# Kernel tuning notes

Measured on AMD Instinct MI355X. Metric: run time of the kernel, lower is better.

## Reference

```python
import jax, jax.numpy as jnp
import numpy as np

B, T = 64, 128
IN, H, L, OUT = 512, 1024, 2, 1


def _gru_scan(seq, Wi, Wh, bi, bh):
    # seq: (S, in_dim); PyTorch GRU cell, gate order r, z, n.
    h0 = jnp.zeros((H,), dtype=seq.dtype)
    def step(h, x):
        gi = x @ Wi.T + bi          # (3H,)
        gh = h @ Wh.T + bh          # (3H,)
        r = jax.nn.sigmoid(gi[:H] + gh[:H])
        z = jax.nn.sigmoid(gi[H:2 * H] + gh[H:2 * H])
        n = jnp.tanh(gi[2 * H:] + r * gh[2 * H:])
        h_new = (1.0 - z) * n + z * h
        return h_new, h_new
    _, hs = jax.lax.scan(step, h0, seq)
    return hs                        # (S, H)


def setup_inputs() -> dict:
    key = jax.random.key(0)
    ks = jax.random.split(key, 24)
    mk = lambda k, shape: jax.random.normal(k, shape, dtype=jnp.float32) * 0.05
    d = {}
    d['x'] = jax.random.normal(ks[0], (B, T, IN), dtype=jnp.float32)
    # gru1: layer0 input=IN, layer1 input=H
    d['g1_Wi0'] = mk(ks[1], (3 * H, IN)); d['g1_Wh0'] = mk(ks[2], (3 * H, H))
    d['g1_bi0'] = mk(ks[3], (3 * H,));    d['g1_bh0'] = mk(ks[4], (3 * H,))
    d['g1_Wi1'] = mk(ks[5], (3 * H, H));  d['g1_Wh1'] = mk(ks[6], (3 * H, H))
    d['g1_bi1'] = mk(ks[7], (3 * H,));    d['g1_bh1'] = mk(ks[8], (3 * H,))
    # gru2: both layers input=H
    d['g2_Wi0'] = mk(ks[9], (3 * H, H));  d['g2_Wh0'] = mk(ks[10], (3 * H, H))
    d['g2_bi0'] = mk(ks[11], (3 * H,));   d['g2_bh0'] = mk(ks[12], (3 * H,))
    d['g2_Wi1'] = mk(ks[13], (3 * H, H)); d['g2_Wh1'] = mk(ks[14], (3 * H, H))
    d['g2_bi1'] = mk(ks[15], (3 * H,));   d['g2_bh1'] = mk(ks[16], (3 * H,))
    d['fc1_W'] = mk(ks[17], (64, H));     d['fc1_b'] = mk(ks[18], (64,))
    d['fc2_W'] = mk(ks[19], (OUT, 64));   d['fc2_b'] = mk(ks[20], (OUT,))
    return d


def reference(x, g1_Wi0, g1_Wh0, g1_bi0, g1_bh0, g1_Wi1, g1_Wh1, g1_bi1, g1_bh1,
              g2_Wi0, g2_Wh0, g2_bi0, g2_bh0, g2_Wi1, g2_Wh1, g2_bi1, g2_bh1,
              fc1_W, fc1_b, fc2_W, fc2_b):
    # PyTorch feeds x[:, t, :] (2-D) to a batch_first GRU -> treated as an
    # UNBATCHED sequence of length B; hidden is carried across t. That equals
    # one GRU scan over the flattened (T*B)-step sequence, t-major / b-minor.
    seq = jnp.swapaxes(x, 0, 1).reshape(T * B, IN)
    hs0 = _gru_scan(seq, g1_Wi0, g1_Wh0, g1_bi0, g1_bh0)    # (T*B, H) layer 0
    hs1 = _gru_scan(hs0, g1_Wi1, g1_Wh1, g1_bi1, g1_bh1)    # (T*B, H) layer 1
    # h returned after timestep t is the hidden at flat step t*B + (B-1)
    s = jnp.stack([hs0, hs1], axis=1)[B - 1::B]             # (T, L, H)
    seq2 = s.reshape(T * L, H)                              # torch.cat(s)
    # gru2 over the [1, T*L, H] sequence (batch=1)
    hs2_0 = _gru_scan(seq2, g2_Wi0, g2_Wh0, g2_bi0, g2_bh0)
    hs2_1 = _gru_scan(hs2_0, g2_Wi1, g2_Wh1, g2_bi1, g2_bh1)
    h2 = jnp.stack([hs2_0[-1], hs2_1[-1]], axis=0)[:, None, :]  # (L, 1, H)
    y = jax.nn.sigmoid(h2 @ fc1_W.T + fc1_b)                # (L, 1, 64)
    out = jax.nn.sigmoid(y @ fc2_W.T + fc2_b)               # (L, 1, OUT)
    return out
```

## Files before the change

kernel.cpp:

```cpp
#include <hip/hip_runtime.h>


typedef unsigned u32x4 __attribute__((ext_vector_type(4)));
typedef unsigned u32x2 __attribute__((ext_vector_type(2)));
typedef _Float16 h2_t  __attribute__((ext_vector_type(2)));

#define NWG 256

__device__ u32x4    g_recL0[2][NWG];
__device__ u32x4    g_recL1[2][NWG];
__device__ unsigned g_seq2[256][512];

__device__ __forceinline__ unsigned pk(float a, float b) {
  unsigned short ua = __builtin_bit_cast(unsigned short, (_Float16)a);
  unsigned short ub = __builtin_bit_cast(unsigned short, (_Float16)b);
  return (unsigned)ua | ((unsigned)ub << 16);
}
__device__ __forceinline__ float unpk(unsigned u, int hi) {
  unsigned short us = (unsigned short)(hi ? (u >> 16) : (u & 0xffffu));
  return (float)__builtin_bit_cast(_Float16, us);
}

#if __has_builtin(__builtin_amdgcn_fdot2)
__device__ __forceinline__ float fdot2(unsigned a, unsigned b, float c) {
  return __builtin_amdgcn_fdot2(__builtin_bit_cast(h2_t, a),
                                __builtin_bit_cast(h2_t, b), c, false);
}
#else
__device__ __forceinline__ float fdot2(unsigned a, unsigned b, float c) {
  h2_t ha = __builtin_bit_cast(h2_t, a), hb = __builtin_bit_cast(h2_t, b);
  return c + (float)ha[0] * (float)hb[0] + (float)ha[1] * (float)hb[1];
}
#endif

__device__ __forceinline__ u32x4 ld_sc_v4(const u32x4* p) {
  u32x4 v;
  asm volatile("global_load_dwordx4 %0, %1, off sc1\n\t"
               "s_waitcnt vmcnt(0)"
               : "=&v"(v) : "v"(p) : "memory");
  return v;
}
__device__ __forceinline__ void st_sc_v4(u32x4* p, u32x4 v) {
  asm volatile("global_store_dwordx4 %0, %1, off sc1"
               :: "v"(p), "v"(v) : "memory");
}
__device__ __forceinline__ void st_sc_v2(void* p, u32x2 v) {
  asm volatile("global_store_dwordx2 %0, %1, off sc1"
               :: "v"(p), "v"(v) : "memory");
}

__device__ __forceinline__ float rcpf(float x) {
#if __has_builtin(__builtin_amdgcn_rcpf)
  return __builtin_amdgcn_rcpf(x);
#else
  return 1.f / x;
#endif
}
__device__ __forceinline__ float sigf(float x) {
  return rcpf(1.f + __expf(-x));
}
__device__ __forceinline__ float tanh_f(float x) {
  x = fminf(fmaxf(x, -15.f), 15.f);
  const float e = __expf(2.f * x);
  return (e - 1.f) * rcpf(e + 1.f);
}

__device__ __forceinline__ int swzHc(int ch) { return ch ^ ((ch >> 3) & 7); }
__device__ __forceinline__ int swzXc(int ch) { return ch ^ ((ch >> 2) & 7); }
__device__ __forceinline__ int swzH_pos(int idx) { return (swzHc(idx >> 2) << 2) | (idx & 3); }
__device__ __forceinline__ int swzX_pos(int idx) { return (swzXc(idx >> 2) << 2) | (idx & 3); }

__global__ void init_recs() {
  int t = blockIdx.x * blockDim.x + threadIdx.x;
  u32x4 ff = {0u, 0u, 0xFFFFFFFFu, 0u};
  if (t < 512)       g_recL0[t >> 8][t & 255] = ff;
  else               g_recL1[(t - 512) >> 8][t & 255] = ff;
}

#define LDROW16(T, A, B, C, D)                                                 \
  {                                                                            \
    const int rr = g4 * 3 + (T);                                               \
    const float4* r4 = (const float4*)(Wm + (size_t)((rr >> 2) * 1024 + j0 +   \
                       (rr & 3)) * cols + kh * (cols >> 1) + q * (cols >> 5)); \
    float4 v;                                                                  \
    v = r4[0]; A[0] = pk(v.x, v.y); A[1] = pk(v.z, v.w);                       \
    v = r4[1]; A[2] = pk(v.x, v.y); A[3] = pk(v.z, v.w);                       \
    v = r4[2]; B[0] = pk(v.x, v.y); B[1] = pk(v.z, v.w);                       \
    v = r4[3]; B[2] = pk(v.x, v.y); B[3] = pk(v.z, v.w);                       \
    v = r4[4]; C[0] = pk(v.x, v.y); C[1] = pk(v.z, v.w);                       \
    v = r4[5]; C[2] = pk(v.x, v.y); C[3] = pk(v.z, v.w);                       \
    v = r4[6]; D[0] = pk(v.x, v.y); D[1] = pk(v.z, v.w);                       \
    v = r4[7]; D[2] = pk(v.x, v.y); D[3] = pk(v.z, v.w);                       \
  }

#define LDROW8(T, A, B)                                                        \
  {                                                                            \
    const int rr = g4 * 3 + (T);                                               \
    const float4* r4 = (const float4*)(Wm + (size_t)((rr >> 2) * 1024 + j0 +   \
                       (rr & 3)) * cols + kh * (cols >> 1) + q * (cols >> 5)); \
    float4 v;                                                                  \
    v = r4[0]; A[0] = pk(v.x, v.y); A[1] = pk(v.z, v.w);                       \
    v = r4[1]; A[2] = pk(v.x, v.y); A[3] = pk(v.z, v.w);                       \
    v = r4[2]; B[0] = pk(v.x, v.y); B[1] = pk(v.z, v.w);                       \
    v = r4[3]; B[2] = pk(v.x, v.y); B[3] = pk(v.z, v.w);                       \
  }

#define DOTK(HSRC, IDX, A, B, C)                                               \
  {                                                                            \
    u32x4 h4 = HSRC[(IDX)];                                                    \
    acc0 = fdot2(A[0], h4[0], acc0); acc0 = fdot2(A[1], h4[1], acc0);          \
    acc0 = fdot2(A[2], h4[2], acc0); acc0 = fdot2(A[3], h4[3], acc0);          \
    acc1 = fdot2(B[0], h4[0], acc1); acc1 = fdot2(B[1], h4[1], acc1);          \
    acc1 = fdot2(B[2], h4[2], acc1); acc1 = fdot2(B[3], h4[3], acc1);          \
    acc2 = fdot2(C[0], h4[0], acc2); acc2 = fdot2(C[1], h4[1], acc2);          \
    acc2 = fdot2(C[2], h4[2], acc2); acc2 = fdot2(C[3], h4[3], acc2);          \
  }

template <int PHASE>
__global__ __launch_bounds__(512, 2) void gru_phase(
    const float* __restrict__ Wm0, const float* __restrict__ Wm1,
    const float* __restrict__ Wm2, const float* __restrict__ Wm3,
    const float* __restrict__ bh0, const float* __restrict__ bi1,
    const float* __restrict__ bh1, const float* __restrict__ bi0,
    const float* __restrict__ x,
    const float* __restrict__ fc1W, const float* __restrict__ fc1b,
    const float* __restrict__ fc2W, const float* __restrict__ fc2b,
    float* __restrict__ out)
{
  constexpr int N0 = (PHASE == 1) ? 8192 : 256;
  constexpr int XC = (PHASE == 1) ? 512 : 1024;

  const int wg   = blockIdx.x;
  const int tid  = threadIdx.x;
  const int wv   = tid >> 6;
  const int lane = tid & 63;
  const int m    = wv >> 1;
  const int kh   = wv & 1;
  const int g4   = lane >> 4;
  const int q    = lane & 15;
  const int j0   = wg * 4;
  const bool m3s = (PHASE == 1) && (m == 3);

  __shared__ __attribute__((aligned(16))) unsigned sH0[2][512];
  __shared__ __attribute__((aligned(16))) unsigned sH1[2][512];
  __shared__ __attribute__((aligned(16))) unsigned sX [2][512];
  __shared__ float sD[2][96];
  __shared__ float sY[128];

  u32x4 W0{}, W1{}, W2{}, W3{}, W4{}, W5{}, W6{}, W7{}, W8{}, W9{}, W10{}, W11{};
  {
    const float* Wm = (m == 0) ? Wm0 : (m == 1) ? Wm1 : (m == 2) ? Wm2 : Wm3;
    const int cols = (m == 3) ? XC : 1024;
    if (m3s) {
      LDROW8(0, W0, W1);
      LDROW8(1, W2, W3);
      LDROW8(2, W4, W5);
    } else {
      LDROW16(0, W0, W4, W8,  W2);
      LDROW16(0, W0, W1, W2,  W3);
      LDROW16(1, W4, W5, W6,  W7);
      LDROW16(2, W8, W9, W10, W11);
    }
  }

  float bI0, bI1, bI2, bH0v, bH1v, bH2v;
  {
    const int i = lane & 3, layer = (lane >> 2) & 1;
    const float* pbi = layer ? bi1 : bi0;
    const float* pbh = layer ? bh1 : bh0;
    bI0 = pbi[0 * 1024 + j0 + i]; bI1 = pbi[1 * 1024 + j0 + i]; bI2 = pbi[2 * 1024 + j0 + i];
    bH0v = pbh[0 * 1024 + j0 + i]; bH1v = pbh[1 * 1024 + j0 + i]; bH2v = pbh[2 * 1024 + j0 + i];
  }

  for (int s = 0; s <= N0; ++s) {
    const int par = s & 1;

    float2 xv = {0.f, 0.f};
    unsigned xs = 0;
    if (PHASE == 1) {
      if (s < N0 && tid < 256) {
        const int b = s & 63, tt = s >> 6;
        xv = ((const float2*)(x + (size_t)(b * 128 + tt) * 512))[tid];
      }
    } else {
      if (s < N0) xs = g_seq2[s][tid];
    }

    const int t2 = tid & 255;
    {
      unsigned d0 = 0, d1 = 0;
      if (s > 0) {
        const unsigned want = (unsigned)(s - 1);
        const u32x4* a = (tid < 256) ? &g_recL0[(s - 1) & 1][t2]
                                     : &g_recL1[(s - 1) & 1][t2];
        u32x4 r = ld_sc_v4(a);
        while (r[2] != want) r = ld_sc_v4(a);
        d0 = r[0]; d1 = r[1];
      }
      unsigned* dst = (tid < 256) ? sH0[par] : sH1[par];
      dst[swzH_pos(2 * t2)]     = d0;
      dst[swzH_pos(2 * t2 + 1)] = d1;
    }
    if (PHASE == 1) {
      if (s < N0 && tid < 256) sX[par][swzX_pos(tid)] = pk(xv.x, xv.y);
    } else {
      if (s < N0) sX[par][swzH_pos(tid)] = xs;
    }
    __syncthreads();

    float acc0 = 0.f, acc1 = 0.f, acc2 = 0.f;
    if (m3s) {
      const u32x4* Xv = (const u32x4*)sX[par];
      const int base = kh * 32 + 2 * q;
      DOTK(Xv, swzXc(base + 0), W0, W2, W4);
      DOTK(Xv, swzXc(base + 1), W1, W3, W5);
    } else {
      const unsigned* hb = (m == 2) ? sH1[par] : (m == 3) ? sX[par] : sH0[par];
      const u32x4* Hv = (const u32x4*)hb;
      const int base = kh * 64 + 4 * q;
      DOTK(Hv, swzHc(base + 0), W0, W4, W8);
      DOTK(Hv, swzHc(base + 1), W1, W5, W9);
      DOTK(Hv, swzHc(base + 2), W2, W6, W10);
      DOTK(Hv, swzHc(base + 3), W3, W7, W11);
    }
    acc0 += __shfl_xor(acc0, 8, 16); acc0 += __shfl_xor(acc0, 4, 16);
    acc0 += __shfl_xor(acc0, 2, 16); acc0 += __shfl_xor(acc0, 1, 16);
    acc1 += __shfl_xor(acc1, 8, 16); acc1 += __shfl_xor(acc1, 4, 16);
    acc1 += __shfl_xor(acc1, 2, 16); acc1 += __shfl_xor(acc1, 1, 16);
    acc2 += __shfl_xor(acc2, 8, 16); acc2 += __shfl_xor(acc2, 4, 16);
    acc2 += __shfl_xor(acc2, 2, 16); acc2 += __shfl_xor(acc2, 1, 16);
    if (q < 3) {
      const float dv = (q == 0) ? acc0 : (q == 1) ? acc1 : acc2;
      sD[par][m * 24 + kh * 12 + g4 * 3 + q] = dv;
    }
    __syncthreads();

    if (wv == 0) {
      const int i = lane & 3;
      const int layer = (lane >> 2) & 1;
      const float* Sd = sD[par];
      const int mI = layer ? 1 : 3;
      const int mH = layer ? 2 : 0;
      const float dIr = Sd[mI * 24 + 0 + i] + Sd[mI * 24 + 12 + 0 + i];
      const float dIz = Sd[mI * 24 + 4 + i] + Sd[mI * 24 + 12 + 4 + i];
      const float dIn = Sd[mI * 24 + 8 + i] + Sd[mI * 24 + 12 + 8 + i];
      const float dHr = Sd[mH * 24 + 0 + i] + Sd[mH * 24 + 12 + 0 + i];
      const float dHz = Sd[mH * 24 + 4 + i] + Sd[mH * 24 + 12 + 4 + i];
      const float dHn = Sd[mH * 24 + 8 + i] + Sd[mH * 24 + 12 + 8 + i];
      const float rg = sigf(dIr + bI0 + dHr + bH0v);
      const float zg = sigf(dIz + bI1 + dHz + bH1v);
      const float ng = tanh_f(dIn + bI2 + rg * (dHn + bH2v));
      const int   jj = 2 * wg + (i >> 1);
      const unsigned hu = (layer ? sH1 : sH0)[par][swzH_pos(jj)];
      const float hp = unpk(hu, i & 1);
      float hn = (1.f - zg) * ng + zg * hp;
      const bool valid = layer ? (s >= 1) : (s < N0);
      hn = valid ? hn : 0.f;
      const float v0 = __shfl(hn, 0), v1 = __shfl(hn, 1);
      const float v2 = __shfl(hn, 2), v3 = __shfl(hn, 3);
      const float w0 = __shfl(hn, 4), w1 = __shfl(hn, 5);
      const float w2 = __shfl(hn, 6), w3 = __shfl(hn, 7);
      if (lane == 0) {
        u32x4 rec0 = {pk(v0, v1), pk(v2, v3), (unsigned)s, 0u};
        u32x4 rec1 = {pk(w0, w1), pk(w2, w3), (unsigned)s, 0u};
        st_sc_v4(&g_recL0[par][wg], rec0);
        st_sc_v4(&g_recL1[par][wg], rec1);
        if (PHASE == 1) {
          if ((s & 63) == 63) {
            u32x2 t2v = {rec0[0], rec0[1]};
            st_sc_v2(&g_seq2[2 * (s >> 6)][2 * wg], t2v);
          }
          if (s >= 1 && ((s - 1) & 63) == 63) {
            u32x2 t2v = {rec1[0], rec1[1]};
            st_sc_v2(&g_seq2[2 * ((s - 1) >> 6) + 1][2 * wg], t2v);
          }
        }
      }
    }
  }

  if (PHASE == 2 && wg == 0) {
    if (tid < 256) {
      const u32x4* a1 = &g_recL1[0][tid];
      u32x4 r1 = ld_sc_v4(a1);
      while (r1[2] != 256u) r1 = ld_sc_v4(a1);
      sH1[0][swzH_pos(2 * tid)]     = r1[0];
      sH1[0][swzH_pos(2 * tid + 1)] = r1[1];
    }
    __syncthreads();
    if (tid < 128) {
      const int lsel = tid >> 6;
      const int k = tid & 63;
      const unsigned* Hs = lsel ? sH1[0] : sH0[0];
      const float* wrow = fc1W + (size_t)k * 1024;
      float a = fc1b[k];
      for (int j2 = 0; j2 < 512; ++j2) {
        const unsigned hu = Hs[swzH_pos(j2)];
        a += unpk(hu, 0) * wrow[2 * j2] + unpk(hu, 1) * wrow[2 * j2 + 1];
      }
      sY[tid] = sigf(a);
    }
    __syncthreads();
    if (tid < 2) {
      const float* yv = sY + tid * 64;
      float a = fc2b[0];
      for (int k2 = 0; k2 < 64; ++k2) a += fc2W[k2] * yv[k2];
      out[tid] = sigf(a);
    }
  }
}

extern "C" void kernel_launch(void* const* d_in, const int* in_sizes, int n_in,
                              void* d_out, int out_size, void* d_ws, size_t ws_size,
                              hipStream_t stream) {
  (void)in_sizes; (void)n_in; (void)out_size; (void)d_ws; (void)ws_size;
  const float* x      = (const float*)d_in[0];
  const float* g1_Wi0 = (const float*)d_in[1];
  const float* g1_Wh0 = (const float*)d_in[2];
  const float* g1_bi0 = (const float*)d_in[3];
  const float* g1_bh0 = (const float*)d_in[4];
  const float* g1_Wi1 = (const float*)d_in[5];
  const float* g1_Wh1 = (const float*)d_in[6];
  const float* g1_bi1 = (const float*)d_in[7];
  const float* g1_bh1 = (const float*)d_in[8];
  const float* g2_Wi0 = (const float*)d_in[9];
  const float* g2_Wh0 = (const float*)d_in[10];
  const float* g2_bi0 = (const float*)d_in[11];
  const float* g2_bh0 = (const float*)d_in[12];
  const float* g2_Wi1 = (const float*)d_in[13];
  const float* g2_Wh1 = (const float*)d_in[14];
  const float* g2_bi1 = (const float*)d_in[15];
  const float* g2_bh1 = (const float*)d_in[16];
  const float* fc1W   = (const float*)d_in[17];
  const float* fc1b   = (const float*)d_in[18];
  const float* fc2W   = (const float*)d_in[19];
  const float* fc2b   = (const float*)d_in[20];
  float* out = (float*)d_out;

  init_recs<<<dim3(4), dim3(256), 0, stream>>>();
  gru_phase<1><<<dim3(NWG), dim3(512), 0, stream>>>(
      g1_Wh0, g1_Wi1, g1_Wh1, g1_Wi0, g1_bh0, g1_bi1, g1_bh1, g1_bi0,
      x, fc1W, fc1b, fc2W, fc2b, out);
  gru_phase<2><<<dim3(NWG), dim3(512), 0, stream>>>(
      g2_Wh0, g2_Wi1, g2_Wh1, g2_Wi0, g2_bh0, g2_bi1, g2_bh1, g2_bi0,
      x, fc1W, fc1b, fc2W, fc2b, out);
}
```

Measured before the change: 26.75 ms.

## Relay cross-step hidden state through one elected block per XCD

Elects one workgroup per XCC with an atomic CAS to act as a relay. The relay polls the system-coherent recurrence buffers and copies the records into a per-XCC mirror held at L2 scope. Other workgroups spin on that L2-local mirror instead, with an occasional fallback poll of the global buffer. The aim is to cut cross-die coherent polling traffic and latency in the per-step barrier, at the cost of an extra hop through the relay and more init work. It also removes a redundant duplicate weight-load macro.

```diff
diff --git a/kernel.cpp b/kernel.cpp
--- a/kernel.cpp
+++ b/kernel.cpp
@@ -9,6 +9,8 @@
 
 __device__ u32x4    g_recL0[2][NWG];
 __device__ u32x4    g_recL1[2][NWG];
+__device__ u32x4    g_mirror[8][2][512];
+__device__ int      g_relay[8];
 __device__ unsigned g_seq2[256][512];
 
 __device__ __forceinline__ unsigned pk(float a, float b) {
@@ -40,8 +42,19 @@
                : "=&v"(v) : "v"(p) : "memory");
   return v;
 }
+__device__ __forceinline__ u32x4 ld_l2_v4(const u32x4* p) {
+  u32x4 v;
+  asm volatile("global_load_dwordx4 %0, %1, off sc0\n\t"
+               "s_waitcnt vmcnt(0)"
+               : "=&v"(v) : "v"(p) : "memory");
+  return v;
+}
 __device__ __forceinline__ void st_sc_v4(u32x4* p, u32x4 v) {
   asm volatile("global_store_dwordx4 %0, %1, off sc1"
+               :: "v"(p), "v"(v) : "memory");
+}
+__device__ __forceinline__ void st_l2_v4(u32x4* p, u32x4 v) {
+  asm volatile("global_store_dwordx4 %0, %1, off sc0"
                :: "v"(p), "v"(v) : "memory");
 }
 __device__ __forceinline__ void st_sc_v2(void* p, u32x2 v) {
@@ -73,8 +86,10 @@
 __global__ void init_recs() {
   int t = blockIdx.x * blockDim.x + threadIdx.x;
   u32x4 ff = {0u, 0u, 0xFFFFFFFFu, 0u};
-  if (t < 512)       g_recL0[t >> 8][t & 255] = ff;
-  else               g_recL1[(t - 512) >> 8][t & 255] = ff;
+  if (t < 512)              g_recL0[t >> 8][t & 255] = ff;
+  else if (t < 1024)        g_recL1[(t - 512) >> 8][t & 255] = ff;
+  else if (t < 1024 + 8192) ((u32x4*)g_mirror)[t - 1024] = ff;
+  if (t < 8) g_relay[t] = -1;
 }
 
 #define LDROW16(T, A, B, C, D)                                                 \
@@ -146,6 +161,15 @@
   __shared__ __attribute__((aligned(16))) unsigned sX [2][512];
   __shared__ float sD[2][96];
   __shared__ float sY[128];
+  __shared__ int   sRole;
+
+  unsigned xcc;
+  asm volatile("s_getreg_b32 %0, hwreg(HW_REG_XCC_ID)" : "=s"(xcc));
+  xcc &= 7u;
+  if (tid == 0) {
+    int old = atomicCAS(&g_relay[xcc], -1, (int)blockIdx.x);
+    sRole = (old == -1) ? 1 : 0;
+  }
 
   u32x4 W0{}, W1{}, W2{}, W3{}, W4{}, W5{}, W6{}, W7{}, W8{}, W9{}, W10{}, W11{};
   {
@@ -156,7 +180,6 @@
       LDROW8(1, W2, W3);
       LDROW8(2, W4, W5);
     } else {
-      LDROW16(0, W0, W4, W8,  W2);
       LDROW16(0, W0, W1, W2,  W3);
       LDROW16(1, W4, W5, W6,  W7);
       LDROW16(2, W8, W9, W10, W11);
@@ -171,6 +194,9 @@
     bI0 = pbi[0 * 1024 + j0 + i]; bI1 = pbi[1 * 1024 + j0 + i]; bI2 = pbi[2 * 1024 + j0 + i];
     bH0v = pbh[0 * 1024 + j0 + i]; bH1v = pbh[1 * 1024 + j0 + i]; bH2v = pbh[2 * 1024 + j0 + i];
   }
+
+  __syncthreads();
+  const bool isRelay = (sRole != 0);
 
   for (int s = 0; s <= N0; ++s) {
     const int par = s & 1;
@@ -191,10 +217,22 @@
       unsigned d0 = 0, d1 = 0;
       if (s > 0) {
         const unsigned want = (unsigned)(s - 1);
-        const u32x4* a = (tid < 256) ? &g_recL0[(s - 1) & 1][t2]
-                                     : &g_recL1[(s - 1) & 1][t2];
-        u32x4 r = ld_sc_v4(a);
-        while (r[2] != want) r = ld_sc_v4(a);
+        const int par2 = (s - 1) & 1;
+        const u32x4* ga = (tid < 256) ? &g_recL0[par2][t2] : &g_recL1[par2][t2];
+        u32x4 r;
+        if (isRelay) {
+          r = ld_sc_v4(ga);
+          while (r[2] != want) r = ld_sc_v4(ga);
+          st_l2_v4(&g_mirror[xcc][par2][tid], r);
+        } else {
+          const u32x4* mp = &g_mirror[xcc][par2][tid];
+          r = ld_l2_v4(mp);
+          int spin = 0;
+          while (r[2] != want) {
+            if (((++spin) & 63) == 0) r = ld_sc_v4(ga);
+            else                      r = ld_l2_v4(mp);
+          }
+        }
         d0 = r[0]; d1 = r[1];
       }
       unsigned* dst = (tid < 256) ? sH0[par] : sH1[par];
@@ -337,10 +375,11 @@
   const float* fc2b   = (const float*)d_in[20];
   float* out = (float*)d_out;
 
-  init_recs<<<dim3(4), dim3(256), 0, stream>>>();
+  init_recs<<<dim3(40), dim3(256), 0, stream>>>();
   gru_phase<1><<<dim3(NWG), dim3(512), 0, stream>>>(
       g1_Wh0, g1_Wi1, g1_Wh1, g1_Wi0, g1_bh0, g1_bi1, g1_bh1, g1_bi0,
       x, fc1W, fc1b, fc2W, fc2b, out);
+  init_recs<<<dim3(40), dim3(256), 0, stream>>>();
   gru_phase<2><<<dim3(NWG), dim3(512), 0, stream>>>(
       g2_Wh0, g2_Wi1, g2_Wh1, g2_Wi0, g2_bh0, g2_bi1, g2_bh1, g2_bi0,
       x, fc1W, fc1b, fc2W, fc2b, out);
```

Result: slower. 61.73 ms (+130.7%).
